# Optimization experiments

Hardware: AMD Instinct MI355X
Metric: run time of the kernel (lower is better)

The kernel has to match this reference:

```python
import jax, jax.numpy as jnp
import numpy as np
from jax import lax

B, NQ, C = 2, 1024, 2048
H, DH = 16, 128
G, CD = 4, 512          # off_grps, off_dim = C // G
LR, HR = 24, 72         # low-res grid side, high-res grid side
INTER = 64
K = LR * LR             # sampled K/V tokens (grid_size == lr_size)


def setup_inputs() -> dict:
    key = jax.random.key(0)
    ks = jax.random.split(key, 16)
    s = 0.02
    d = {}
    d['hidden_states'] = jax.random.normal(ks[0], (B, NQ, C), jnp.float32)
    d['image_hd'] = jax.random.normal(ks[1], (B, HR * HR, C), jnp.float32)
    d['wq'] = jax.random.normal(ks[2], (C, C), jnp.float32) * s
    d['wk'] = jax.random.normal(ks[3], (C, C), jnp.float32) * s
    d['wv'] = jax.random.normal(ks[4], (C, C), jnp.float32) * s
    d['wo'] = jax.random.normal(ks[5], (C, C), jnp.float32) * s
    d['conv_dw_w'] = jax.random.normal(ks[6], (CD, 1, 3, 3), jnp.float32) * s
    d['ln1_w'] = jnp.ones((CD,), jnp.float32)
    d['ln1_b'] = jnp.zeros((CD,), jnp.float32)
    d['conv_lr_proj_w'] = jax.random.normal(ks[7], (INTER, CD), jnp.float32) * s
    d['proj_int_w'] = jax.random.normal(ks[8], (INTER, CD), jnp.float32) * s
    d['proj_int_b'] = jnp.zeros((INTER,), jnp.float32)
    d['ln2_w'] = jnp.ones((INTER,), jnp.float32)
    d['ln2_b'] = jnp.zeros((INTER,), jnp.float32)
    d['conv_off_w'] = jax.random.normal(ks[9], (2, INTER), jnp.float32) * s
    d['k_hd_w'] = jax.random.normal(ks[10], (C, C), jnp.float32) * s
    d['k_hd_b'] = jnp.zeros((C,), jnp.float32)
    d['v_hd_w'] = jax.random.normal(ks[11], (C, C), jnp.float32) * s
    d['v_hd_b'] = jnp.zeros((C,), jnp.float32)
    return d


def _ln_channels(x, w, b, eps=1e-5):
    # LayerNorm2d: normalize over channel axis of [N, C, H, W]
    mu = jnp.mean(x, axis=1, keepdims=True)
    var = jnp.var(x, axis=1, keepdims=True)
    xn = (x - mu) * lax.rsqrt(var + eps)
    return xn * w[None, :, None, None] + b[None, :, None, None]


def _tokens_to_grid(x, S):
    # [B, S*S, C] -> [B*G, CD, S, S]  (group channels like einops '(b) (h w) (g c) -> (b g) c h w')
    return x.reshape(B, S, S, G, CD).transpose(0, 3, 4, 1, 2).reshape(B * G, CD, S, S)


def _bilinear_sample(img, grid):
    # img [N, C, Hh, Wh]; grid [N, K, 2] (x, y) normalized to [-1, 1], align_corners=True
    N, Cc, Hh, Wh = img.shape
    x = (grid[..., 0] + 1.0) * 0.5 * (Wh - 1)
    y = (grid[..., 1] + 1.0) * 0.5 * (Hh - 1)
    x0f, y0f = jnp.floor(x), jnp.floor(y)
    wx = (x - x0f)[:, None, :]
    wy = (y - y0f)[:, None, :]
    x0 = jnp.clip(x0f.astype(jnp.int32), 0, Wh - 1)
    x1 = jnp.clip(x0 + 1, 0, Wh - 1)
    y0 = jnp.clip(y0f.astype(jnp.int32), 0, Hh - 1)
    y1 = jnp.clip(y0 + 1, 0, Hh - 1)
    imgf = img.reshape(N, Cc, Hh * Wh)
    gather = jax.vmap(lambda im, ix: im[:, ix])  # ([C,HW],[K]) -> [C,K]
    v00 = gather(imgf, y0 * Wh + x0)
    v01 = gather(imgf, y0 * Wh + x1)
    v10 = gather(imgf, y1 * Wh + x0)
    v11 = gather(imgf, y1 * Wh + x1)
    return (v00 * (1 - wx) * (1 - wy) + v01 * wx * (1 - wy)
            + v10 * (1 - wx) * wy + v11 * wx * wy)  # [N, C, K]


def _ref_grid():
    # normalized reference points as in _grid_generate (centers / (S-1) * 2 - 1)
    yy = (jnp.linspace(0.5, LR - 0.5, LR) / (LR - 1.0)) * 2.0 - 1.0
    xx = (jnp.linspace(0.5, LR - 0.5, LR) / (LR - 1.0)) * 2.0 - 1.0
    gy, gx = jnp.meshgrid(yy, xx, indexing='ij')
    return jnp.stack([gx, gy], axis=-1).reshape(K, 2)  # (x, y)


def reference(hidden_states, image_hd, wq, wk, wv, wo, conv_dw_w, ln1_w, ln1_b,
              conv_lr_proj_w, proj_int_w, proj_int_b, ln2_w, ln2_b, conv_off_w,
              k_hd_w, k_hd_b, v_hd_w, v_hd_b):
    # ---- QKV on the full sequence ----
    q = hidden_states @ wq.T
    k_txt = hidden_states @ wk.T
    v_txt = hidden_states @ wv.T

    # ---- offset network on LR image tokens (first LR*LR tokens) ----
    lr = _tokens_to_grid(hidden_states[:, :K, :], LR)          # [B*G, CD, LR, LR]
    x = lax.conv_general_dilated(lr, conv_dw_w, (1, 1), 'SAME',
                                 feature_group_count=CD,
                                 dimension_numbers=('NCHW', 'OIHW', 'NCHW'))
    x = jax.nn.silu(x)
    x = _ln_channels(x, ln1_w, ln1_b)
    x = jnp.einsum('nchw,oc->nohw', x, conv_lr_proj_w)          # 1x1 conv -> [B*G, INTER, LR, LR]
    # intention gate from spatially pooled group features
    pooled = jnp.mean(lr, axis=(2, 3))                          # [B*G, CD]
    gate = jax.nn.sigmoid(pooled @ proj_int_w.T + proj_int_b)   # [B*G, INTER]
    x = x * gate[:, :, None, None]
    x = _ln_channels(x, ln2_w, ln2_b)
    off = jnp.einsum('nchw,oc->nohw', x, conv_off_w)            # [B*G, 2, LR, LR]
    off = off.transpose(0, 2, 3, 1).reshape(B * G, K, 2)        # (x, y)
    pos = jnp.tanh(_ref_grid()[None] + off)                     # sampling locs in [-1, 1]

    # ---- deformable gather from HD features ----
    hd = _tokens_to_grid(image_hd, HR)                          # [B*G, CD, HR, HR]
    samp = _bilinear_sample(hd, pos)                            # [B*G, CD, K]
    samp = samp.reshape(B, G, CD, K).transpose(0, 3, 1, 2).reshape(B, K, C)
    k_hd = samp @ k_hd_w.T + k_hd_b
    v_hd = samp @ v_hd_w.T + v_hd_b

    # ---- attention: causal over text tokens, HD tokens fully visible ----
    k_all = jnp.concatenate([k_txt, k_hd], axis=1)              # [B, NQ+K, C]
    v_all = jnp.concatenate([v_txt, v_hd], axis=1)
    qh = q.reshape(B, NQ, H, DH).transpose(0, 2, 1, 3)
    kh = k_all.reshape(B, NQ + K, H, DH).transpose(0, 2, 1, 3)
    vh = v_all.reshape(B, NQ + K, H, DH).transpose(0, 2, 1, 3)
    scores = jnp.einsum('bhqd,bhkd->bhqk', qh, kh) / jnp.sqrt(jnp.float32(DH))
    col = jnp.arange(NQ + K)
    row = jnp.arange(NQ)
    allow = (col[None, :] >= NQ) | (col[None, :] <= row[:, None])
    scores = jnp.where(allow[None, None], scores, jnp.float32(-1e9))
    attn = jax.nn.softmax(scores, axis=-1)
    out = jnp.einsum('bhqk,bhkd->bhqd', attn, vh)
    out = out.transpose(0, 2, 1, 3).reshape(B, NQ, C)
    return out @ wo.T
```

## Files before the change

kernel.cpp:

```cpp
#include <hip/hip_runtime.h>

typedef unsigned short u16;
typedef unsigned int u32;
typedef __attribute__((ext_vector_type(8))) short bf8;
typedef __attribute__((ext_vector_type(4))) float f4;
typedef __attribute__((ext_vector_type(4))) unsigned short us4;

constexpr int B = 2;
constexpr int NQ = 1024;
constexpr int C = 2048;
constexpr int DH = 128;
constexpr int G = 4;
constexpr int CD = 512;
constexpr int LR = 24;
constexpr int HR = 72;
constexpr int INTER = 64;
constexpr int K = LR * LR;
constexpr int NKV = NQ + K;

#define MFMA16(a, b, c) __builtin_amdgcn_mfma_f32_16x16x32_bf16(a, b, c, 0, 0, 0)
#define GLDS(g, l)                                                         \
  __builtin_amdgcn_global_load_lds(                                        \
      (const __attribute__((address_space(1))) void*)(g),                  \
      (__attribute__((address_space(3))) void*)(l), 16, 0, 0)
#define SB()                               \
  do {                                     \
    __builtin_amdgcn_sched_barrier(0);     \
    __builtin_amdgcn_s_barrier();          \
    __builtin_amdgcn_sched_barrier(0);     \
  } while (0)
#define WVM(n)                                              \
  do {                                                      \
    asm volatile("s_waitcnt vmcnt(" #n ")" ::: "memory");   \
    __builtin_amdgcn_sched_barrier(0);                      \
  } while (0)

__device__ __forceinline__ u16 f2bf1(float f) {
  u32 u = __float_as_uint(f);
  u32 r = (u + 0x7fffu + ((u >> 16) & 1u)) >> 16;
  return (u16)r;
}

__global__ __launch_bounds__(256) void f2bf_k9(
    const float* __restrict__ s0, const float* __restrict__ s1,
    const float* __restrict__ s2, const float* __restrict__ s3,
    const float* __restrict__ s4, const float* __restrict__ s5,
    const float* __restrict__ s6, const float* __restrict__ plrw,
    const float* __restrict__ cdw, u16* __restrict__ d0, u16* __restrict__ d1,
    u16* __restrict__ d2, u16* __restrict__ d3, u16* __restrict__ d4,
    u16* __restrict__ d5, u16* __restrict__ d6, float* __restrict__ wt,
    float* __restrict__ x1, float* __restrict__ pooled) {
  __shared__ float SH[32 * 577];
  const int y = blockIdx.y;
  const int t = threadIdx.x;
  if (y == 7) {
    if (blockIdx.x >= 128) return;
    const int idx = blockIdx.x * 256 + t;
    wt[idx] = plrw[(idx & 63) * 512 + (idx >> 6)];
    return;
  }
  if (y == 8) {
    if (blockIdx.x >= 128) return;
    const int n = blockIdx.x >> 4, cg = blockIdx.x & 15;
    const int b = n >> 2, g = n & 3;
    const int c0 = cg * 32;
    {
      const int c = t & 31, pr = t >> 5;
      const float* src = s0 + (size_t)b * 1024 * 2048 + g * 512 + c0 + c;
#pragma unroll 4
      for (int j = 0; j < 72; ++j) {
        const int p = j * 8 + pr;
        SH[c * 577 + p] = src[(size_t)p * 2048];
      }
    }
    __syncthreads();
    {
      const int c = t >> 3, seg = t & 7;
      float s = 0.f;
      for (int i = 0; i < 72; ++i) s += SH[c * 577 + seg * 72 + i];
      s += __shfl_xor(s, 1);
      s += __shfl_xor(s, 2);
      s += __shfl_xor(s, 4);
      if (seg == 0) pooled[n * 512 + c0 + c] = s * (1.f / 576.f);
    }
    const size_t base_out = (size_t)(n * 512 + c0) * 576;
    for (int j = 0; j < 72; ++j) {
      const int idx = j * 256 + t;
      const int c = idx / 576, p = idx - c * 576;
      const int yy0 = p / 24, xx0 = p - yy0 * 24;
      const float* wp = cdw + (c0 + c) * 9;
      float s = 0.f;
#pragma unroll
      for (int dy = -1; dy <= 1; ++dy)
#pragma unroll
        for (int dx = -1; dx <= 1; ++dx) {
          const int yy = yy0 + dy, xx = xx0 + dx;
          if (yy < 0 || yy >= 24 || xx < 0 || xx >= 24) continue;
          s += SH[c * 577 + yy * 24 + xx] * wp[(dy + 1) * 3 + dx + 1];
        }
      x1[base_out + idx] = s / (1.f + expf(-s));
    }
    return;
  }
  const float* s;
  u16* d;
  switch (y) {
    case 0: s = s0; d = d0; break;
    case 1: s = s1; d = d1; break;
    case 2: s = s2; d = d2; break;
    case 3: s = s3; d = d3; break;
    case 4: s = s4; d = d4; break;
    case 5: s = s5; d = d5; break;
    default: s = s6; d = d6; break;
  }
  if (y < 5) {
    u16* L = (u16*)SH;
    const int pc = blockIdx.x;
    const int mb = pc >> 5, kb = pc & 31;
    const int rin = t >> 2, c0 = (t & 3) * 16;
    const float* src = s + (size_t)(mb * 64 + rin) * 2048 + kb * 64 + c0;
#pragma unroll
    for (int j = 0; j < 16; j += 4) {
      float4 v = *(const float4*)(src + j);
      L[rin * 68 + c0 + j] = f2bf1(v.x);
      L[rin * 68 + c0 + j + 1] = f2bf1(v.y);
      L[rin * 68 + c0 + j + 2] = f2bf1(v.z);
      L[rin * 68 + c0 + j + 3] = f2bf1(v.w);
    }
    __syncthreads();
    u16* dst = d + (size_t)pc * 4096 + t * 16;
#pragma unroll
    for (int gg = 0; gg < 2; ++gg) {
      const int g = t * 2 + gg;
      const int rh = g & 15, ks2 = (g >> 4) & 3, kc = (g >> 6) & 1, fr = g >> 7;
      const int row = fr * 16 + rh, cc = kc * 32 + ks2 * 8;
      us4 o0, o1;
      o0.x = L[row * 68 + cc];     o0.y = L[row * 68 + cc + 1];
      o0.z = L[row * 68 + cc + 2]; o0.w = L[row * 68 + cc + 3];
      o1.x = L[row * 68 + cc + 4]; o1.y = L[row * 68 + cc + 5];
      o1.z = L[row * 68 + cc + 6]; o1.w = L[row * 68 + cc + 7];
      *(us4*)(dst + gg * 8) = o0;
      *(us4*)(dst + gg * 8 + 4) = o1;
    }
  } else {
    const size_t i0 = ((size_t)blockIdx.x * 256 + t) * 16;
#pragma unroll
    for (int j = 0; j < 16; j += 4) {
      float4 v = *(const float4*)(s + i0 + j);
      us4 o;
      o.x = f2bf1(v.x); o.y = f2bf1(v.y); o.z = f2bf1(v.z); o.w = f2bf1(v.w);
      *(us4*)(d + i0 + j) = o;
    }
  }
}

__global__ __launch_bounds__(512, 2) void gemm_fused(
    const u16* __restrict__ Ast, const u16* __restrict__ Wq,
    const u16* __restrict__ Wk, const u16* __restrict__ Wv,
    const u16* __restrict__ samp, const u16* __restrict__ khw,
    const u16* __restrict__ vhw, const float* __restrict__ khb,
    const float* __restrict__ vhb, u16* __restrict__ outq,
    u16* __restrict__ kg, u16* __restrict__ vg) {
  __shared__ u16 As[2][4][4096];
  __shared__ u16 Bs[2][4][4096];
  const int tid = threadIdx.x, lane = tid & 63, w = tid >> 6;
  const int ks = lane >> 4, r = lane & 15;
  const int bid = blockIdx.x;

  if (bid < 192) {
    const int wm = w >> 2, wn = w & 3;
    const int swz = (bid & 7) * 24 + (bid >> 3);
    const int mt = swz / 24, nt = swz % 24;
    const u16* Wst = (nt < 8) ? Wq : (nt < 16) ? Wk : Wv;
    const int nb0 = (nt & 7) * 4;
    const int mb0 = mt * 4;

#define ST_A03(bi, kt)                                                        \
  do {                                                                        \
    GLDS(Ast + ((size_t)(mb0 + 0) * 32 + (kt)) * 4096 + tid * 8,              \
         &As[bi][0][tid * 8]);                                                \
    GLDS(Ast + ((size_t)(mb0 + 2) * 32 + (kt)) * 4096 + tid * 8,              \
         &As[bi][2][tid * 8]);                                                \
  } while (0)
#define ST_A47(bi, kt)                                                        \
  do {                                                                        \
    GLDS(Ast + ((size_t)(mb0 + 1) * 32 + (kt)) * 4096 + tid * 8,              \
         &As[bi][1][tid * 8]);                                                \
    GLDS(Ast + ((size_t)(mb0 + 3) * 32 + (kt)) * 4096 + tid * 8,              \
         &As[bi][3][tid * 8]);                                                \
  } while (0)
#define ST_B01(bi, kt)                                                        \
  do {                                                                        \
    GLDS(Wst + ((size_t)(nb0 + 0) * 32 + (kt)) * 4096 + tid * 8,              \
         &Bs[bi][0][tid * 8]);                                                \
    GLDS(Wst + ((size_t)(nb0 + 1) * 32 + (kt)) * 4096 + tid * 8,              \
         &Bs[bi][1][tid * 8]);                                                \
  } while (0)
#define ST_B23(bi, kt)                                                        \
  do {                                                                        \
    GLDS(Wst + ((size_t)(nb0 + 2) * 32 + (kt)) * 4096 + tid * 8,              \
         &Bs[bi][2][tid * 8]);                                                \
    GLDS(Wst + ((size_t)(nb0 + 3) * 32 + (kt)) * 4096 + tid * 8,              \
         &Bs[bi][3][tid * 8]);                                                \
  } while (0)
#define RD_A(dst, bi, half, kc)                                               \
  _Pragma("unroll") for (int i2 = 0; i2 < 4; ++i2) dst[i2] =                  \
      *(const bf8*)(&As[bi][wm * 2 + (half)]                                  \
                       [((i2 * 2 + (kc)) * 4 + ks) * 128 + r * 8]);
#define RD_B(dst, bi, kc)                                                     \
  _Pragma("unroll") for (int j2 = 0; j2 < 4; ++j2) dst[j2] =                  \
      *(const bf8*)(&Bs[bi][wn][((j2 * 2 + (kc)) * 4 + ks) * 128 + r * 8]);
#define MM(ACC, AF, BF)                                                       \
  do {                                                                        \
    __builtin_amdgcn_s_setprio(1);                                            \
    _Pragma("unroll") for (int i3 = 0; i3 < 4; ++i3)                          \
        _Pragma("unroll") for (int j3 = 0; j3 < 4; ++j3) ACC[i3][j3] =        \
            MFMA16(AF[i3], BF[j3], ACC[i3][j3]);                              \
    __builtin_amdgcn_s_setprio(0);                                            \
  } while (0)

    f4 accA[4][4], accB[4][4];
#pragma unroll
    for (int i = 0; i < 4; ++i)
#pragma unroll
      for (int j = 0; j < 4; ++j) {
        accA[i][j] = f4{0.f, 0.f, 0.f, 0.f};
        accB[i][j] = f4{0.f, 0.f, 0.f, 0.f};
      }
    bf8 af[4], b0[4], b1[4];

    ST_A03(0, 0); ST_B01(0, 0); ST_B23(0, 0); ST_A47(0, 0);
    ST_A03(1, 1); ST_B01(1, 1);
    WVM(6);
    SB();

    for (int t = 0; t < 32; ++t) {
      const int buf = t & 1;
      RD_A(af, buf, 0, 0);
      RD_B(b0, buf, 0);
      if (t + 1 < 32) ST_B23(buf ^ 1, t + 1);
      SB();
      MM(accA, af, b0);
      SB();
      RD_A(af, buf, 0, 1);
      RD_B(b1, buf, 1);
      if (t + 1 < 32) ST_A47(buf ^ 1, t + 1);
      SB();
      MM(accA, af, b1);
      if (t + 1 < 32) { WVM(8); } else { WVM(0); }
      SB();
      RD_A(af, buf, 1, 0);
      if (t + 2 < 32) ST_A03(buf, t + 2);
      SB();
      MM(accB, af, b0);
      SB();
      RD_A(af, buf, 1, 1);
      if (t + 2 < 32) ST_B01(buf, t + 2);
      SB();
      MM(accB, af, b1);
      if (t + 2 < 32) { WVM(6); } else if (t + 1 < 32) { WVM(2); }
      SB();
    }

#define EPI(ACC, HALF)                                                        \
  _Pragma("unroll") for (int i = 0; i < 4; ++i)                               \
      _Pragma("unroll") for (int j = 0; j < 4; ++j)                           \
          _Pragma("unroll") for (int rr = 0; rr < 4; ++rr) {                  \
    const int m = mt * 256 + wm * 128 + (HALF)*64 + i * 16 + ks * 4 + rr;     \
    const int n = nt * 256 + wn * 64 + j * 16 + r;                            \
    const float v = ACC[i][j][rr];                                            \
    const int sel = n >> 11, nn = n & 2047, hh = nn >> 7, dd = nn & 127;      \
    const int bb = m >> 10, qq = m & 1023;                                    \
    const u16 bv = f2bf1(v);                                                  \
    if (sel == 0) {                                                           \
      outq[(size_t)m * 2048 + nn] = bv;                                       \
    } else if (sel == 1) {                                                    \
      kg[(((size_t)(bb * 16 + hh) * 50 + (qq >> 5)) * 16 + (dd >> 3)) * 256 + \
         (qq & 31) * 8 + (dd & 7)] = bv;                                      \
    } else {                                                                  \
      vg[((size_t)(bb * 16 + hh) * 200 + (qq >> 3)) * 1024 + dd * 8 +         \
         (qq & 7)] = bv;                                                      \
    }                                                                         \
  }
    EPI(accA, 0)
    EPI(accB, 1)
#undef EPI
  } else {
    const int hb = bid - 192;
    const int mt = hb >> 4, nb = hb & 15;
    const int m0 = mt * 128, n0l = nb * 128;
    const int srow = lane >> 2, scol = (lane & 3) * 8;
    const int wh = w & 3;
    const int wr = wh >> 1, wc = wh & 1;
    const bool is_v = (w >= 4);
    const u16* Wp = is_v ? vhw : khw;
    const float* bias = is_v ? vhb : khb;

#define HDST(bi, k0)                                                          \
  do {                                                                        \
    GLDS(samp + (size_t)(m0 + w * 16 + srow) * 2048 + scol + (k0),            \
         &As[bi][0][w * 512 + lane * 8]);                                     \
    GLDS(Wp + (size_t)(n0l + wh * 32 + srow) * 2048 + scol + (k0),            \
         &Bs[bi][is_v ? 1 : 0][wh * 1024 + lane * 8]);                        \
    GLDS(Wp + (size_t)(n0l + wh * 32 + 16 + srow) * 2048 + scol + (k0),       \
         &Bs[bi][is_v ? 1 : 0][wh * 1024 + 512 + lane * 8]);                  \
  } while (0)

    f4 acc[4][4];
#pragma unroll
    for (int i = 0; i < 4; ++i)
#pragma unroll
      for (int j = 0; j < 4; ++j) acc[i][j] = f4{0.f, 0.f, 0.f, 0.f};
    const int koff = ks * 8;
    const int arow = wr * 64 + r, brow = wc * 64 + r;

    HDST(0, 0);
    int cur = 0;
    for (int k0 = 0; k0 < 2048; k0 += 32) {
      SB();
      if (k0 + 32 < 2048) {
        HDST(cur ^ 1, k0 + 32);
        WVM(3);
      } else {
        WVM(0);
      }
      SB();
      bf8 af2[4], bw[4];
#pragma unroll
      for (int i = 0; i < 4; ++i)
        af2[i] = *(const bf8*)(&As[cur][0][(arow + i * 16) * 32 + koff]);
#pragma unroll
      for (int j = 0; j < 4; ++j)
        bw[j] =
            *(const bf8*)(&Bs[cur][is_v ? 1 : 0][(brow + j * 16) * 32 + koff]);
      __builtin_amdgcn_s_setprio(1);
#pragma unroll
      for (int i = 0; i < 4; ++i)
#pragma unroll
        for (int j = 0; j < 4; ++j)
          acc[i][j] = MFMA16(af2[i], bw[j], acc[i][j]);
      __builtin_amdgcn_s_setprio(0);
      cur ^= 1;
    }
#undef HDST
    const int rbase = ks * 4;
#pragma unroll
    for (int i = 0; i < 4; ++i) {
#pragma unroll
      for (int j = 0; j < 4; ++j) {
        const int nn = n0l + wc * 64 + j * 16 + r;
        const int hh = nn >> 7, dd = nn & 127;
#pragma unroll
        for (int rr = 0; rr < 4; ++rr) {
          const int m = m0 + wr * 64 + i * 16 + rbase + rr;
          const int bb = m / 576;
          const int kv = 1024 + (m - bb * 576);
          const u16 bv = f2bf1(acc[i][j][rr] + bias[nn]);
          if (!is_v) {
            kg[(((size_t)(bb * 16 + hh) * 50 + (kv >> 5)) * 16 + (dd >> 3)) *
                   256 +
               (kv & 31) * 8 + (dd & 7)] = bv;
          } else {
            vg[((size_t)(bb * 16 + hh) * 200 + (kv >> 3)) * 1024 + dd * 8 +
               (kv & 7)] = bv;
          }
        }
      }
    }
  }
}

__global__ __launch_bounds__(256) void gemm_out_st(const u16* __restrict__ Ast2,
                                                   const u16* __restrict__ Wst,
                                                   float* __restrict__ outf) {
  __shared__ u16 As2[2][2][4096];
  __shared__ u16 Ws2[2][2][4096];
  const int tid = threadIdx.x, lane = tid & 63, w = tid >> 6;
  const int wr = w >> 1, wc = w & 1;
  const int ks = lane >> 4, r = lane & 15;
  const int mt = blockIdx.y, nt = blockIdx.x;

#define OST(bi, kt)                                                           \
  do {                                                                        \
    const size_t a0 = ((size_t)(mt * 2 + 0) * 32 + (kt)) * 4096;              \
    const size_t a1 = ((size_t)(mt * 2 + 1) * 32 + (kt)) * 4096;              \
    const size_t w0 = ((size_t)(nt * 2 + 0) * 32 + (kt)) * 4096;              \
    const size_t w1 = ((size_t)(nt * 2 + 1) * 32 + (kt)) * 4096;              \
    GLDS(Ast2 + a0 + tid * 8, &As2[bi][0][tid * 8]);                          \
    GLDS(Ast2 + a0 + 2048 + tid * 8, &As2[bi][0][2048 + tid * 8]);            \
    GLDS(Ast2 + a1 + tid * 8, &As2[bi][1][tid * 8]);                          \
    GLDS(Ast2 + a1 + 2048 + tid * 8, &As2[bi][1][2048 + tid * 8]);            \
    GLDS(Wst + w0 + tid * 8, &Ws2[bi][0][tid * 8]);                           \
    GLDS(Wst + w0 + 2048 + tid * 8, &Ws2[bi][0][2048 + tid * 8]);             \
    GLDS(Wst + w1 + tid * 8, &Ws2[bi][1][tid * 8]);                           \
    GLDS(Wst + w1 + 2048 + tid * 8, &Ws2[bi][1][2048 + tid * 8]);             \
  } while (0)

  f4 acc[4][4];
#pragma unroll
  for (int i = 0; i < 4; ++i)
#pragma unroll
    for (int j = 0; j < 4; ++j) acc[i][j] = f4{0.f, 0.f, 0.f, 0.f};

  OST(0, 0);
  int cur = 0;
  for (int kt = 0; kt < 32; ++kt) {
    SB();
    if (kt + 1 < 32) {
      OST(cur ^ 1, kt + 1);
      WVM(8);
    } else {
      WVM(0);
    }
    SB();
#pragma unroll
    for (int kc = 0; kc < 2; ++kc) {
      bf8 a_[4], b_[4];
#pragma unroll
      for (int i = 0; i < 4; ++i)
        a_[i] = *(const bf8*)(&As2[cur][wr][((i * 2 + kc) * 4 + ks) * 128 +
                                            r * 8]);
#pragma unroll
      for (int j = 0; j < 4; ++j)
        b_[j] = *(const bf8*)(&Ws2[cur][wc][((j * 2 + kc) * 4 + ks) * 128 +
                                            r * 8]);
      __builtin_amdgcn_s_setprio(1);
#pragma unroll
      for (int i = 0; i < 4; ++i)
#pragma unroll
        for (int j = 0; j < 4; ++j)
          acc[i][j] = MFMA16(a_[i], b_[j], acc[i][j]);
      __builtin_amdgcn_s_setprio(0);
    }
    cur ^= 1;
  }
#undef OST
#pragma unroll
  for (int i = 0; i < 4; ++i)
#pragma unroll
    for (int j = 0; j < 4; ++j) {
      const int n = nt * 128 + wc * 64 + j * 16 + r;
#pragma unroll
      for (int rr = 0; rr < 4; ++rr) {
        const int m = mt * 128 + wr * 64 + i * 16 + ks * 4 + rr;
        outf[(size_t)m * 2048 + n] = acc[i][j][rr];
      }
    }
}

__global__ __launch_bounds__(256) void lnproj_gate(
    const float* __restrict__ x1, const float* __restrict__ ln1w,
    const float* __restrict__ ln1b, const float* __restrict__ wt,
    const float* __restrict__ pooled, const float* __restrict__ piw,
    const float* __restrict__ pib, float* __restrict__ x2,
    float* __restrict__ gate) {
  __shared__ float Xs[512][68];
  __shared__ float rs[4][64], rss[4][64];
  const int bidx = blockIdx.x;
  const int t = threadIdx.x;
  if (bidx >= 72) {
    const int idx = (bidx - 72) * 256 + t;
    const int n = idx >> 6, o = idx & 63;
    const float* pb = pooled + n * 512;
    const float* wb = piw + o * 512;
    float s = pib[o];
    for (int c = 0; c < 512; ++c) s += pb[c] * wb[c];
    gate[idx] = 1.f / (1.f + expf(-s));
    return;
  }
  const int n = bidx / 9, pc = bidx % 9;
  const int p0 = pc * 64;
  {
    const int pl = t & 63, c4 = t >> 6;
    const float* src = x1 + (size_t)n * 512 * 576 + p0 + pl;
#pragma unroll 4
    for (int j = 0; j < 128; ++j) {
      const int c = j * 4 + c4;
      Xs[c][pl] = src[(size_t)c * 576];
    }
  }
  __syncthreads();
  {
    const int pl = t & 63, q = t >> 6;
    float s = 0.f, ss = 0.f;
    for (int c = q * 128; c < q * 128 + 128; ++c) {
      const float v = Xs[c][pl];
      s += v;
      ss += v * v;
    }
    rs[q][pl] = s;
    rss[q][pl] = ss;
    __syncthreads();
    const float S = rs[0][pl] + rs[1][pl] + rs[2][pl] + rs[3][pl];
    const float SS = rss[0][pl] + rss[1][pl] + rss[2][pl] + rss[3][pl];
    const float mean = S * (1.f / 512.f);
    const float inv = rsqrtf(SS * (1.f / 512.f) - mean * mean + 1e-5f);
    for (int c = q * 128; c < q * 128 + 128; ++c)
      Xs[c][pl] = (Xs[c][pl] - mean) * inv * ln1w[c] + ln1b[c];
  }
  __syncthreads();
  {
    const int o4 = (t & 15) * 4, pl0 = (t >> 4) * 4;
    float acc[4][4] = {};
    for (int c = 0; c < 512; ++c) {
      const f4 xv = *(const f4*)(&Xs[c][pl0]);
      const f4 wv = *(const f4*)(&wt[c * 64 + o4]);
#pragma unroll
      for (int i = 0; i < 4; ++i)
#pragma unroll
        for (int j = 0; j < 4; ++j) acc[i][j] += wv[i] * xv[j];
    }
#pragma unroll
    for (int i = 0; i < 4; ++i) {
      f4 ov;
      ov[0] = acc[i][0]; ov[1] = acc[i][1];
      ov[2] = acc[i][2]; ov[3] = acc[i][3];
      *(f4*)(&x2[(size_t)(n * 64 + o4 + i) * 576 + p0 + pl0]) = ov;
    }
  }
}

__global__ __launch_bounds__(256) void pos_sample(
    const float* __restrict__ x2, const float* __restrict__ gate,
    const float* __restrict__ ln2w, const float* __restrict__ ln2b,
    const float* __restrict__ offw, const float* __restrict__ img,
    u16* __restrict__ samp) {
  const int bk = blockIdx.x;
  const int b = bk / K, k = bk % K;
  __shared__ int s_idx[G][4];
  __shared__ float s_w[G][4];
  const int t = threadIdx.x;
  const int g = t >> 6, lane = t & 63;
  {
    const int n = b * G + g;
    float v = x2[((size_t)n * INTER + lane) * K + k] * gate[n * INTER + lane];
    float s = v, ss = v * v;
    for (int o = 32; o; o >>= 1) {
      s += __shfl_xor(s, o);
      ss += __shfl_xor(ss, o);
    }
    const float mean = s * (1.f / INTER);
    const float var = ss * (1.f / INTER) - mean * mean;
    const float xn = (v - mean) * rsqrtf(var + 1e-5f) * ln2w[lane] + ln2b[lane];
    float ox = xn * offw[lane];
    float oy = xn * offw[INTER + lane];
    for (int o = 32; o; o >>= 1) {
      ox += __shfl_xor(ox, o);
      oy += __shfl_xor(oy, o);
    }
    if (lane == 0) {
      const int yi = k / LR, xi = k % LR;
      const float rx = (xi + 0.5f) / 23.f * 2.f - 1.f;
      const float ry = (yi + 0.5f) / 23.f * 2.f - 1.f;
      const float px = tanhf(rx + ox), py = tanhf(ry + oy);
      const float x = (px + 1.f) * 0.5f * (HR - 1);
      const float y = (py + 1.f) * 0.5f * (HR - 1);
      const float x0f = floorf(x), y0f = floorf(y);
      const float wx = x - x0f, wy = y - y0f;
      const int x0 = min(max((int)x0f, 0), HR - 1);
      const int x1 = min(x0 + 1, HR - 1);
      const int y0 = min(max((int)y0f, 0), HR - 1);
      const int y1 = min(y0 + 1, HR - 1);
      s_idx[g][0] = y0 * HR + x0;
      s_idx[g][1] = y0 * HR + x1;
      s_idx[g][2] = y1 * HR + x0;
      s_idx[g][3] = y1 * HR + x1;
      s_w[g][0] = (1.f - wx) * (1.f - wy);
      s_w[g][1] = wx * (1.f - wy);
      s_w[g][2] = (1.f - wx) * wy;
      s_w[g][3] = wx * wy;
    }
  }
  __syncthreads();
  const float* ib = img + (size_t)b * HR * HR * C;
  u16* ob = samp + ((size_t)b * K + k) * C;
  for (int ch = t; ch < C; ch += 256) {
    const int gg = ch >> 9;
    float v = s_w[gg][0] * ib[(size_t)s_idx[gg][0] * C + ch] +
              s_w[gg][1] * ib[(size_t)s_idx[gg][1] * C + ch] +
              s_w[gg][2] * ib[(size_t)s_idx[gg][2] * C + ch] +
              s_w[gg][3] * ib[(size_t)s_idx[gg][3] * C + ch];
    ob[ch] = f2bf1(v);
  }
}

__global__ __launch_bounds__(256) void attn_part(
    const u16* __restrict__ qb, const u16* __restrict__ kg,
    const u16* __restrict__ vg, float* __restrict__ oA,
    float* __restrict__ oB, float* __restrict__ mlA,
    float* __restrict__ mlB) {
  const int i = blockIdx.x;
  const int fam = i >> 9;
  const int r9 = i & 511;
  int bh, qblk;
  if (fam == 0) {
    const int pair = r9 & 255, half = r9 >> 8;
    bh = pair & 31;
    const int q8 = pair >> 5;
    qblk = half ? (15 - q8) : q8;
  } else {
    bh = r9 & 31;
    qblk = r9 >> 5;
  }
  const int b = bh >> 4, h = bh & 15;
  const int q0 = qblk * 64;
  const int tid = threadIdx.x, lane = tid & 63, w = tid >> 6;
  const int qw = q0 + w * 16;
  const int col = lane & 15, kpart = lane >> 4, rbase = kpart * 4;
  __shared__ u16 Ks[2][4096];
  __shared__ u16 Vs[2][4096];
  __shared__ u16 Pl[4][16 * 40];
  float* oacc = fam ? oB : oA;
  float* ml = fam ? mlB : mlA;
  bf8 qf[4];
  {
    const u16* qp =
        qb + (size_t)(b * 1024 + qw + col) * 2048 + h * 128 + kpart * 8;
#pragma unroll
    for (int dc = 0; dc < 4; ++dc) qf[dc] = *(const bf8*)(qp + dc * 32);
  }
  f4 o[8];
#pragma unroll
  for (int df = 0; df < 8; ++df) o[df] = f4{0.f, 0.f, 0.f, 0.f};
  float m_r[4] = {-1e30f, -1e30f, -1e30f, -1e30f};
  float l_p[4] = {0.f, 0.f, 0.f, 0.f};
  const float scale = 0.08838834764831845f;
  const int nt = fam ? 18 : ((q0 + 64) >> 5);
  const int kvadd = fam ? 1024 : 0;
  const u16* kbh = kg + (size_t)bh * (NKV * 128);
  const u16* vbh = vg + (size_t)bh * (NKV * 128);
  u16* pw = &Pl[w][0];

#define ASTAGE(bi, kv0)                                                       \
  do {                                                                        \
    const u16* gk = kbh + (size_t)((kv0) >> 5) * 4096 + w * 1024 + lane * 8;  \
    GLDS(gk, &Ks[bi][w * 1024 + lane * 8]);                                   \
    GLDS(gk + 512, &Ks[bi][w * 1024 + 512 + lane * 8]);                       \
    const u16* gv = vbh + (size_t)((kv0) >> 3) * 1024 + w * 1024 + lane * 8;  \
    GLDS(gv, &Vs[bi][w * 1024 + lane * 8]);                                   \
    GLDS(gv + 512, &Vs[bi][w * 1024 + 512 + lane * 8]);                       \
  } while (0)

  ASTAGE(0, kvadd);
  int cur = 0;
  for (int t = 0; t < nt; ++t) {
    const int kv0 = kvadd + (t << 5);
    SB();
    if (t + 1 < nt) {
      ASTAGE(cur ^ 1, kvadd + ((t + 1) << 5));
      WVM(4);
    } else {
      WVM(0);
    }
    SB();
    const u16* ksb = &Ks[cur][0];
    const u16* vsb = &Vs[cur][0];
    f4 s0 = {0.f, 0.f, 0.f, 0.f}, s1 = {0.f, 0.f, 0.f, 0.f};
    __builtin_amdgcn_s_setprio(1);
#pragma unroll
    for (int dc = 0; dc < 4; ++dc) {
      const int dblk = dc * 4 + kpart;
      bf8 k0f = *(const bf8*)(ksb + (dblk * 32 + col) * 8);
      bf8 k1f = *(const bf8*)(ksb + (dblk * 32 + 16 + col) * 8);
      s0 = MFMA16(qf[dc], k0f, s0);
      s1 = MFMA16(qf[dc], k1f, s1);
    }
    __builtin_amdgcn_s_setprio(0);
    float sa[4], sc[4], loc[4], p0[4], p1[4];
    bool grow = false;
    const bool need_mask = (fam == 0) && (kv0 + 31 > qw);
#pragma unroll
    for (int rr = 0; rr < 4; ++rr) {
      float a = s0[rr] * scale, c2 = s1[rr] * scale;
      if (need_mask) {
        const int qg = qw + rbase + rr;
        if (kv0 + col > qg) a = -1e30f;
        if (kv0 + 16 + col > qg) c2 = -1e30f;
      }
      sa[rr] = a; sc[rr] = c2;
      loc[rr] = fmaxf(a, c2);
      grow |= (loc[rr] > m_r[rr] + 8.f);
    }
    if (__any(grow)) {
      float fr[4];
#pragma unroll
      for (int rr = 0; rr < 4; ++rr) {
        float mx = loc[rr];
        mx = fmaxf(mx, __shfl_xor(mx, 1));
        mx = fmaxf(mx, __shfl_xor(mx, 2));
        mx = fmaxf(mx, __shfl_xor(mx, 4));
        mx = fmaxf(mx, __shfl_xor(mx, 8));
        const float mn = fmaxf(m_r[rr], mx);
        fr[rr] = __expf(m_r[rr] - mn);
        m_r[rr] = mn;
        p0[rr] = __expf(sa[rr] - mn);
        p1[rr] = __expf(sc[rr] - mn);
        l_p[rr] = l_p[rr] * fr[rr] + p0[rr] + p1[rr];
      }
#pragma unroll
      for (int df = 0; df < 8; ++df) {
        o[df][0] *= fr[0]; o[df][1] *= fr[1];
        o[df][2] *= fr[2]; o[df][3] *= fr[3];
      }
    } else {
#pragma unroll
      for (int rr = 0; rr < 4; ++rr) {
        p0[rr] = __expf(sa[rr] - m_r[rr]);
        p1[rr] = __expf(sc[rr] - m_r[rr]);
        l_p[rr] += p0[rr] + p1[rr];
      }
    }
#pragma unroll
    for (int rr = 0; rr < 4; ++rr) {
      pw[(rbase + rr) * 40 + col] = f2bf1(p0[rr]);
      pw[(rbase + rr) * 40 + 16 + col] = f2bf1(p1[rr]);
    }
    bf8 pa = *(const bf8*)(pw + col * 40 + kpart * 8);
    __builtin_amdgcn_s_setprio(1);
#pragma unroll
    for (int df = 0; df < 8; ++df) {
      bf8 vf = *(const bf8*)(vsb + (kpart * 128 + df * 16 + col) * 8);
      o[df] = MFMA16(pa, vf, o[df]);
    }
    __builtin_amdgcn_s_setprio(0);
    cur ^= 1;
  }
#undef ASTAGE
  float l_r[4];
#pragma unroll
  for (int rr = 0; rr < 4; ++rr) {
    float ps = l_p[rr];
    ps += __shfl_xor(ps, 1);
    ps += __shfl_xor(ps, 2);
    ps += __shfl_xor(ps, 4);
    ps += __shfl_xor(ps, 8);
    l_r[rr] = ps;
  }
  float* orow = oacc + (size_t)(bh * 1024 + qw + rbase) * 128 + col;
#pragma unroll
  for (int df = 0; df < 8; ++df)
#pragma unroll
    for (int rr = 0; rr < 4; ++rr)
      orow[(size_t)rr * 128 + df * 16] = o[df][rr];
  if (col == 0) {
#pragma unroll
    for (int rr = 0; rr < 4; ++rr) {
      const int row = bh * 1024 + qw + rbase + rr;
      ml[row * 2] = m_r[rr];
      ml[row * 2 + 1] = l_r[rr];
    }
  }
}

__global__ __launch_bounds__(256) void attn_merge(
    const float* __restrict__ oA, const float* __restrict__ mlA,
    const float* __restrict__ oB, const float* __restrict__ mlB,
    u16* __restrict__ aob_st) {
  const int gid = blockIdx.x * 256 + threadIdx.x;
  const int row = gid >> 5;
  const int d0 = (gid & 31) * 4;
  const float mA = mlA[row * 2], lA = mlA[row * 2 + 1];
  const float mB = mlB[row * 2], lB = mlB[row * 2 + 1];
  const float m = fmaxf(mA, mB);
  const float wA = __expf(mA - m), wB = __expf(mB - m);
  const float inv = 1.f / (lA * wA + lB * wB);
  const f4 a = *(const f4*)(oA + (size_t)row * 128 + d0);
  const f4 c = *(const f4*)(oB + (size_t)row * 128 + d0);
  const int bh = row >> 10, q = row & 1023;
  const int bb = bh >> 4, h = bh & 15;
  const int mm = bb * 1024 + q;
  const int col = h * 128 + d0;
  const int mb = mm >> 6, fr = (mm >> 4) & 3, r = mm & 15;
  const int kb = col >> 6, kc = (col >> 5) & 1, ks = (col >> 3) & 3,
            j0 = col & 7;
  u16* dst = aob_st + ((size_t)(mb * 32 + kb)) * 4096 +
             (((fr * 2 + kc) * 4 + ks) * 16 + r) * 8 + j0;
  us4 ov;
  ov.x = f2bf1((a[0] * wA + c[0] * wB) * inv);
  ov.y = f2bf1((a[1] * wA + c[1] * wB) * inv);
  ov.z = f2bf1((a[2] * wA + c[2] * wB) * inv);
  ov.w = f2bf1((a[3] * wA + c[3] * wB) * inv);
  *(us4*)dst = ov;
}

extern "C" void kernel_launch(void* const* d_in, const int* in_sizes, int n_in,
                              void* d_out, int out_size, void* d_ws,
                              size_t ws_size, hipStream_t stream) {
  const float* hs = (const float*)d_in[0];
  const float* img = (const float*)d_in[1];
  const float* wq = (const float*)d_in[2];
  const float* wk = (const float*)d_in[3];
  const float* wv = (const float*)d_in[4];
  const float* wo = (const float*)d_in[5];
  const float* cdw = (const float*)d_in[6];
  const float* ln1w = (const float*)d_in[7];
  const float* ln1b = (const float*)d_in[8];
  const float* plrw = (const float*)d_in[9];
  const float* piw = (const float*)d_in[10];
  const float* pib = (const float*)d_in[11];
  const float* ln2w = (const float*)d_in[12];
  const float* ln2b = (const float*)d_in[13];
  const float* offw = (const float*)d_in[14];
  const float* khw = (const float*)d_in[15];
  const float* khb = (const float*)d_in[16];
  const float* vhw = (const float*)d_in[17];
  const float* vhb = (const float*)d_in[18];
  float* outp = (float*)d_out;

  u16* wsp = (u16*)d_ws;
  const size_t SZ = 4194304;
  u16* hs_st = wsp;
  u16* wq_st = wsp + SZ;
  u16* wk_st = wsp + 2 * SZ;
  u16* wv_st = wsp + 3 * SZ;
  u16* wo_st = wsp + 4 * SZ;
  u16* khw_bf = wsp + 5 * SZ;
  u16* vhw_bf = wsp + 6 * SZ;
  u16* qb_bf = wsp + 7 * SZ;
  u16* samp_bf = wsp + 8 * SZ;
  u16* kg = wsp + 8 * SZ + 2359296;
  u16* vg = kg + 6553600;
  float* x1b = (float*)kg + 2359296;
  float* x2b = x1b + 2359296;
  float* poolb = x2b + 294912;
  float* gb = poolb + 4096;
  float* posb = (float*)(vg + 6553600);
  float* mlA = posb + 9216;
  float* mlB = mlA + 65536;
  float* wtb = mlB + 65536;
  float* oA = (float*)(wsp + 2 * SZ);
  float* oB = (float*)(wsp + 5 * SZ);
  u16* aob_st = wq_st;

  dim3 blk(256);
  f2bf_k9<<<dim3(1024, 9), blk, 0, stream>>>(
      hs, wq, wk, wv, wo, khw, vhw, plrw, cdw, hs_st, wq_st, wk_st, wv_st,
      wo_st, khw_bf, vhw_bf, wtb, x1b, poolb);
  lnproj_gate<<<dim3(74), blk, 0, stream>>>(x1b, ln1w, ln1b, wtb, poolb, piw,
                                            pib, x2b, gb);
  pos_sample<<<dim3(B * K), blk, 0, stream>>>(x2b, gb, ln2w, ln2b, offw, img,
                                              samp_bf);
  gemm_fused<<<dim3(336), dim3(512), 0, stream>>>(
      hs_st, wq_st, wk_st, wv_st, samp_bf, khw_bf, vhw_bf, khb, vhb, qb_bf,
      kg, vg);
  attn_part<<<dim3(1024), blk, 0, stream>>>(qb_bf, kg, vg, oA, oB, mlA, mlB);
  attn_merge<<<dim3(4096), blk, 0, stream>>>(oA, mlA, oB, mlB, aob_st);
  gemm_out_st<<<dim3(16, 16), blk, 0, stream>>>(aob_st, wo_st, outp);
}
```

Baseline: 346.1 us.

## Unify GEMMs into one templated tile kernel and fuse attention halves

Replaces the 512-thread 256x256 QKV GEMM and separate HD and output GEMMs with a single templated 256-thread, 128x128-tile kernel that uses XCD-aware block mapping. All weights, including the HD K/V weights, are now pre-staged into the swizzled tile layout, and the sampler writes directly in that layout. Attention now processes text and HD keys in one pass per block, which removes the split partial outputs and the separate merge kernel. The aim is fewer launches, less intermediate fp32 traffic and better load balance, at the cost of smaller tiles with less operand reuse and longer per-block attention loops.

Result: slower. 420.7 us (+21.5%).

```diff
diff --git a/kernel.cpp b/kernel.cpp
--- a/kernel.cpp
+++ b/kernel.cpp
@@ -113,246 +113,175 @@
     case 5: s = s5; d = d5; break;
     default: s = s6; d = d6; break;
   }
-  if (y < 5) {
-    u16* L = (u16*)SH;
-    const int pc = blockIdx.x;
-    const int mb = pc >> 5, kb = pc & 31;
-    const int rin = t >> 2, c0 = (t & 3) * 16;
-    const float* src = s + (size_t)(mb * 64 + rin) * 2048 + kb * 64 + c0;
-#pragma unroll
-    for (int j = 0; j < 16; j += 4) {
-      float4 v = *(const float4*)(src + j);
-      L[rin * 68 + c0 + j] = f2bf1(v.x);
-      L[rin * 68 + c0 + j + 1] = f2bf1(v.y);
-      L[rin * 68 + c0 + j + 2] = f2bf1(v.z);
-      L[rin * 68 + c0 + j + 3] = f2bf1(v.w);
-    }
-    __syncthreads();
-    u16* dst = d + (size_t)pc * 4096 + t * 16;
-#pragma unroll
-    for (int gg = 0; gg < 2; ++gg) {
-      const int g = t * 2 + gg;
-      const int rh = g & 15, ks2 = (g >> 4) & 3, kc = (g >> 6) & 1, fr = g >> 7;
-      const int row = fr * 16 + rh, cc = kc * 32 + ks2 * 8;
-      us4 o0, o1;
-      o0.x = L[row * 68 + cc];     o0.y = L[row * 68 + cc + 1];
-      o0.z = L[row * 68 + cc + 2]; o0.w = L[row * 68 + cc + 3];
-      o1.x = L[row * 68 + cc + 4]; o1.y = L[row * 68 + cc + 5];
-      o1.z = L[row * 68 + cc + 6]; o1.w = L[row * 68 + cc + 7];
-      *(us4*)(dst + gg * 8) = o0;
-      *(us4*)(dst + gg * 8 + 4) = o1;
-    }
-  } else {
-    const size_t i0 = ((size_t)blockIdx.x * 256 + t) * 16;
-#pragma unroll
-    for (int j = 0; j < 16; j += 4) {
-      float4 v = *(const float4*)(s + i0 + j);
-      us4 o;
-      o.x = f2bf1(v.x); o.y = f2bf1(v.y); o.z = f2bf1(v.z); o.w = f2bf1(v.w);
-      *(us4*)(d + i0 + j) = o;
-    }
+  u16* L = (u16*)SH;
+  const int pc = blockIdx.x;
+  const int mb = pc >> 5, kb = pc & 31;
+  const int rin = t >> 2, c0 = (t & 3) * 16;
+  const float* src = s + (size_t)(mb * 64 + rin) * 2048 + kb * 64 + c0;
+#pragma unroll
+  for (int j = 0; j < 16; j += 4) {
+    float4 v = *(const float4*)(src + j);
+    L[rin * 68 + c0 + j] = f2bf1(v.x);
+    L[rin * 68 + c0 + j + 1] = f2bf1(v.y);
+    L[rin * 68 + c0 + j + 2] = f2bf1(v.z);
+    L[rin * 68 + c0 + j + 3] = f2bf1(v.w);
+  }
+  __syncthreads();
+  u16* dst = d + (size_t)pc * 4096 + t * 16;
+#pragma unroll
+  for (int gg = 0; gg < 2; ++gg) {
+    const int g = t * 2 + gg;
+    const int rh = g & 15, ks2 = (g >> 4) & 3, kc = (g >> 6) & 1, fr = g >> 7;
+    const int row = fr * 16 + rh, cc = kc * 32 + ks2 * 8;
+    us4 o0, o1;
+    o0.x = L[row * 68 + cc];     o0.y = L[row * 68 + cc + 1];
+    o0.z = L[row * 68 + cc + 2]; o0.w = L[row * 68 + cc + 3];
+    o1.x = L[row * 68 + cc + 4]; o1.y = L[row * 68 + cc + 5];
+    o1.z = L[row * 68 + cc + 6]; o1.w = L[row * 68 + cc + 7];
+    *(us4*)(dst + gg * 8) = o0;
+    *(us4*)(dst + gg * 8 + 4) = o1;
   }
 }
 
-__global__ __launch_bounds__(512, 2) void gemm_fused(
-    const u16* __restrict__ Ast, const u16* __restrict__ Wq,
-    const u16* __restrict__ Wk, const u16* __restrict__ Wv,
-    const u16* __restrict__ samp, const u16* __restrict__ khw,
+template <int MODE>
+__global__ __launch_bounds__(256) void gemm_all(
+    const u16* __restrict__ Ast, const u16* __restrict__ W0,
+    const u16* __restrict__ W1, const u16* __restrict__ W2,
+    const u16* __restrict__ sampst, const u16* __restrict__ khw,
     const u16* __restrict__ vhw, const float* __restrict__ khb,
     const float* __restrict__ vhb, u16* __restrict__ outq,
-    u16* __restrict__ kg, u16* __restrict__ vg) {
-  __shared__ u16 As[2][4][4096];
-  __shared__ u16 Bs[2][4][4096];
+    u16* __restrict__ kg, u16* __restrict__ vg, float* __restrict__ outf) {
+  __shared__ u16 As[2][4096];
+  __shared__ u16 Bs[2][4096];
   const int tid = threadIdx.x, lane = tid & 63, w = tid >> 6;
-  const int ks = lane >> 4, r = lane & 15;
-  const int bid = blockIdx.x;
-
-  if (bid < 192) {
-    const int wm = w >> 2, wn = w & 3;
-    const int swz = (bid & 7) * 24 + (bid >> 3);
-    const int mt = swz / 24, nt = swz % 24;
-    const u16* Wst = (nt < 8) ? Wq : (nt < 16) ? Wk : Wv;
-    const int nb0 = (nt & 7) * 4;
-    const int mb0 = mt * 4;
-
-#define ST_A03(bi, kt)                                                        \
-  do {                                                                        \
-    GLDS(Ast + ((size_t)(mb0 + 0) * 32 + (kt)) * 4096 + tid * 8,              \
-         &As[bi][0][tid * 8]);                                                \
-    GLDS(Ast + ((size_t)(mb0 + 2) * 32 + (kt)) * 4096 + tid * 8,              \
-         &As[bi][2][tid * 8]);                                                \
+  const int wr = w >> 1, wc = w & 1;
+  const int ksl = lane >> 4, rl = lane & 15;
+  int mt, nt;
+  const u16 *Ap, *Wp;
+  bool isHD = false;
+  if (MODE == 0) {
+    if (blockIdx.x < 768) {
+      const int xcd = blockIdx.x & 7, idx = blockIdx.x >> 3;
+      mt = (xcd >> 2) * 8 + idx / 12;
+      nt = (xcd & 3) * 12 + idx % 12;
+      Ap = Ast;
+      Wp = (nt < 16) ? W0 : (nt < 32) ? W1 : W2;
+    } else {
+      isHD = true;
+      const int hb = blockIdx.x - 768, xcd = hb & 7, idx = hb >> 3;
+      mt = idx >> 2;
+      nt = xcd * 4 + (idx & 3);
+      Ap = sampst;
+      Wp = (nt < 16) ? khw : vhw;
+    }
+  } else {
+    const int xcd = blockIdx.x & 7, idx = blockIdx.x >> 3;
+    mt = (xcd >> 2) * 8 + idx / 4;
+    nt = (xcd & 3) * 4 + idx % 4;
+    Ap = Ast;
+    Wp = W0;
+  }
+  const int ma0 = mt * 2;
+  const int nb0 = (nt & 15) * 2;
+
+#define GST(dstArr, srcBase, tb0, kt)                                      \
+  do {                                                                     \
+    const int kb_ = (kt) >> 1, kc_ = (kt) & 1;                             \
+    _Pragma("unroll") for (int r2 = 0; r2 < 2; ++r2) {                     \
+      const int run = r2 * 4 + w;                                          \
+      GLDS(srcBase + ((size_t)((tb0) + (run >> 2)) * 32 + kb_) * 4096 +    \
+               (run & 3) * 1024 + kc_ * 512 + lane * 8,                    \
+           &dstArr[run * 512 + lane * 8]);                                 \
+    }                                                                      \
   } while (0)
-#define ST_A47(bi, kt)                                                        \
-  do {                                                                        \
-    GLDS(Ast + ((size_t)(mb0 + 1) * 32 + (kt)) * 4096 + tid * 8,              \
-         &As[bi][1][tid * 8]);                                                \
-    GLDS(Ast + ((size_t)(mb0 + 3) * 32 + (kt)) * 4096 + tid * 8,              \
-         &As[bi][3][tid * 8]);                                                \
-  } while (0)
-#define ST_B01(bi, kt)                                                        \
-  do {                                                                        \
-    GLDS(Wst + ((size_t)(nb0 + 0) * 32 + (kt)) * 4096 + tid * 8,              \
-         &Bs[bi][0][tid * 8]);                                                \
-    GLDS(Wst + ((size_t)(nb0 + 1) * 32 + (kt)) * 4096 + tid * 8,              \
-         &Bs[bi][1][tid * 8]);                                                \
-  } while (0)
-#define ST_B23(bi, kt)                                                        \
-  do {                                                                        \
-    GLDS(Wst + ((size_t)(nb0 + 2) * 32 + (kt)) * 4096 + tid * 8,              \
-         &Bs[bi][2][tid * 8]);                                                \
-    GLDS(Wst + ((size_t)(nb0 + 3) * 32 + (kt)) * 4096 + tid * 8,              \
-         &Bs[bi][3][tid * 8]);                                                \
-  } while (0)
-#define RD_A(dst, bi, half, kc)                                               \
-  _Pragma("unroll") for (int i2 = 0; i2 < 4; ++i2) dst[i2] =                  \
-      *(const bf8*)(&As[bi][wm * 2 + (half)]                                  \
-                       [((i2 * 2 + (kc)) * 4 + ks) * 128 + r * 8]);
-#define RD_B(dst, bi, kc)                                                     \
-  _Pragma("unroll") for (int j2 = 0; j2 < 4; ++j2) dst[j2] =                  \
-      *(const bf8*)(&Bs[bi][wn][((j2 * 2 + (kc)) * 4 + ks) * 128 + r * 8]);
-#define MM(ACC, AF, BF)                                                       \
-  do {                                                                        \
-    __builtin_amdgcn_s_setprio(1);                                            \
-    _Pragma("unroll") for (int i3 = 0; i3 < 4; ++i3)                          \
-        _Pragma("unroll") for (int j3 = 0; j3 < 4; ++j3) ACC[i3][j3] =        \
-            MFMA16(AF[i3], BF[j3], ACC[i3][j3]);                              \
-    __builtin_amdgcn_s_setprio(0);                                            \
-  } while (0)
-
-    f4 accA[4][4], accB[4][4];
+
+  f4 acc[4][4];
+#pragma unroll
+  for (int i = 0; i < 4; ++i)
+#pragma unroll
+    for (int j = 0; j < 4; ++j) acc[i][j] = f4{0.f, 0.f, 0.f, 0.f};
+
+  GST(As[0], Ap, ma0, 0);
+  GST(Bs[0], Wp, nb0, 0);
+  int cur = 0;
+  for (int kt = 0; kt < 64; ++kt) {
+    SB();
+    if (kt + 1 < 64) {
+      GST(As[cur ^ 1], Ap, ma0, kt + 1);
+      GST(Bs[cur ^ 1], Wp, nb0, kt + 1);
+      WVM(4);
+    } else {
+      WVM(0);
+    }
+    SB();
+    bf8 af[4], bw[4];
 #pragma unroll
     for (int i = 0; i < 4; ++i)
+      af[i] = *(const bf8*)(&As[cur][(wr * 4 + i) * 512 + ksl * 128 + rl * 8]);
+#pragma unroll
+    for (int j = 0; j < 4; ++j)
+      bw[j] = *(const bf8*)(&Bs[cur][(wc * 4 + j) * 512 + ksl * 128 + rl * 8]);
+    __builtin_amdgcn_s_setprio(1);
+#pragma unroll
+    for (int i = 0; i < 4; ++i)
+#pragma unroll
+      for (int j = 0; j < 4; ++j)
+        acc[i][j] = MFMA16(af[i], bw[j], acc[i][j]);
+    __builtin_amdgcn_s_setprio(0);
+    cur ^= 1;
+  }
+#undef GST
+
+  const int rbase = ksl * 4;
+  if (MODE == 1) {
+#pragma unroll
+    for (int i = 0; i < 4; ++i)
 #pragma unroll
       for (int j = 0; j < 4; ++j) {
-        accA[i][j] = f4{0.f, 0.f, 0.f, 0.f};
-        accB[i][j] = f4{0.f, 0.f, 0.f, 0.f};
-      }
-    bf8 af[4], b0[4], b1[4];
-
-    ST_A03(0, 0); ST_B01(0, 0); ST_B23(0, 0); ST_A47(0, 0);
-    ST_A03(1, 1); ST_B01(1, 1);
-    WVM(6);
-    SB();
-
-    for (int t = 0; t < 32; ++t) {
-      const int buf = t & 1;
-      RD_A(af, buf, 0, 0);
-      RD_B(b0, buf, 0);
-      if (t + 1 < 32) ST_B23(buf ^ 1, t + 1);
-      SB();
-      MM(accA, af, b0);
-      SB();
-      RD_A(af, buf, 0, 1);
-      RD_B(b1, buf, 1);
-      if (t + 1 < 32) ST_A47(buf ^ 1, t + 1);
-      SB();
-      MM(accA, af, b1);
-      if (t + 1 < 32) { WVM(8); } else { WVM(0); }
-      SB();
-      RD_A(af, buf, 1, 0);
-      if (t + 2 < 32) ST_A03(buf, t + 2);
-      SB();
-      MM(accB, af, b0);
-      SB();
-      RD_A(af, buf, 1, 1);
-      if (t + 2 < 32) ST_B01(buf, t + 2);
-      SB();
-      MM(accB, af, b1);
-      if (t + 2 < 32) { WVM(6); } else if (t + 1 < 32) { WVM(2); }
-      SB();
-    }
-
-#define EPI(ACC, HALF)                                                        \
-  _Pragma("unroll") for (int i = 0; i < 4; ++i)                               \
-      _Pragma("unroll") for (int j = 0; j < 4; ++j)                           \
-          _Pragma("unroll") for (int rr = 0; rr < 4; ++rr) {                  \
-    const int m = mt * 256 + wm * 128 + (HALF)*64 + i * 16 + ks * 4 + rr;     \
-    const int n = nt * 256 + wn * 64 + j * 16 + r;                            \
-    const float v = ACC[i][j][rr];                                            \
-    const int sel = n >> 11, nn = n & 2047, hh = nn >> 7, dd = nn & 127;      \
-    const int bb = m >> 10, qq = m & 1023;                                    \
-    const u16 bv = f2bf1(v);                                                  \
-    if (sel == 0) {                                                           \
-      outq[(size_t)m * 2048 + nn] = bv;                                       \
-    } else if (sel == 1) {                                                    \
-      kg[(((size_t)(bb * 16 + hh) * 50 + (qq >> 5)) * 16 + (dd >> 3)) * 256 + \
-         (qq & 31) * 8 + (dd & 7)] = bv;                                      \
-    } else {                                                                  \
-      vg[((size_t)(bb * 16 + hh) * 200 + (qq >> 3)) * 1024 + dd * 8 +         \
-         (qq & 7)] = bv;                                                      \
-    }                                                                         \
-  }
-    EPI(accA, 0)
-    EPI(accB, 1)
-#undef EPI
+        const int n = nt * 128 + wc * 64 + j * 16 + rl;
+#pragma unroll
+        for (int rr = 0; rr < 4; ++rr) {
+          const int m = mt * 128 + wr * 64 + i * 16 + rbase + rr;
+          outf[(size_t)m * 2048 + n] = acc[i][j][rr];
+        }
+      }
+  } else if (!isHD) {
+    const int sel = nt >> 4;
+#pragma unroll
+    for (int i = 0; i < 4; ++i)
+#pragma unroll
+      for (int j = 0; j < 4; ++j) {
+        const int n2 = (nt & 15) * 128 + wc * 64 + j * 16 + rl;
+        const int hh = n2 >> 7, dd = n2 & 127;
+#pragma unroll
+        for (int rr = 0; rr < 4; ++rr) {
+          const int m = mt * 128 + wr * 64 + i * 16 + rbase + rr;
+          const int bb = m >> 10, qq = m & 1023;
+          const u16 bv = f2bf1(acc[i][j][rr]);
+          if (sel == 0) {
+            outq[(size_t)m * 2048 + n2] = bv;
+          } else if (sel == 1) {
+            kg[(((size_t)(bb * 16 + hh) * 50 + (qq >> 5)) * 16 + (dd >> 3)) *
+                   256 +
+               (qq & 31) * 8 + (dd & 7)] = bv;
+          } else {
+            vg[((size_t)(bb * 16 + hh) * 200 + (qq >> 3)) * 1024 + dd * 8 +
+               (qq & 7)] = bv;
+          }
+        }
+      }
   } else {
-    const int hb = bid - 192;
-    const int mt = hb >> 4, nb = hb & 15;
-    const int m0 = mt * 128, n0l = nb * 128;
-    const int srow = lane >> 2, scol = (lane & 3) * 8;
-    const int wh = w & 3;
-    const int wr = wh >> 1, wc = wh & 1;
-    const bool is_v = (w >= 4);
-    const u16* Wp = is_v ? vhw : khw;
+    const bool is_v = (nt >= 16);
     const float* bias = is_v ? vhb : khb;
-
-#define HDST(bi, k0)                                                          \
-  do {                                                                        \
-    GLDS(samp + (size_t)(m0 + w * 16 + srow) * 2048 + scol + (k0),            \
-         &As[bi][0][w * 512 + lane * 8]);                                     \
-    GLDS(Wp + (size_t)(n0l + wh * 32 + srow) * 2048 + scol + (k0),            \
-         &Bs[bi][is_v ? 1 : 0][wh * 1024 + lane * 8]);                        \
-    GLDS(Wp + (size_t)(n0l + wh * 32 + 16 + srow) * 2048 + scol + (k0),       \
-         &Bs[bi][is_v ? 1 : 0][wh * 1024 + 512 + lane * 8]);                  \
-  } while (0)
-
-    f4 acc[4][4];
 #pragma unroll
     for (int i = 0; i < 4; ++i)
 #pragma unroll
-      for (int j = 0; j < 4; ++j) acc[i][j] = f4{0.f, 0.f, 0.f, 0.f};
-    const int koff = ks * 8;
-    const int arow = wr * 64 + r, brow = wc * 64 + r;
-
-    HDST(0, 0);
-    int cur = 0;
-    for (int k0 = 0; k0 < 2048; k0 += 32) {
-      SB();
-      if (k0 + 32 < 2048) {
-        HDST(cur ^ 1, k0 + 32);
-        WVM(3);
-      } else {
-        WVM(0);
-      }
-      SB();
-      bf8 af2[4], bw[4];
-#pragma unroll
-      for (int i = 0; i < 4; ++i)
-        af2[i] = *(const bf8*)(&As[cur][0][(arow + i * 16) * 32 + koff]);
-#pragma unroll
-      for (int j = 0; j < 4; ++j)
-        bw[j] =
-            *(const bf8*)(&Bs[cur][is_v ? 1 : 0][(brow + j * 16) * 32 + koff]);
-      __builtin_amdgcn_s_setprio(1);
-#pragma unroll
-      for (int i = 0; i < 4; ++i)
-#pragma unroll
-        for (int j = 0; j < 4; ++j)
-          acc[i][j] = MFMA16(af2[i], bw[j], acc[i][j]);
-      __builtin_amdgcn_s_setprio(0);
-      cur ^= 1;
-    }
-#undef HDST
-    const int rbase = ks * 4;
-#pragma unroll
-    for (int i = 0; i < 4; ++i) {
-#pragma unroll
       for (int j = 0; j < 4; ++j) {
-        const int nn = n0l + wc * 64 + j * 16 + r;
+        const int nn = (nt & 15) * 128 + wc * 64 + j * 16 + rl;
         const int hh = nn >> 7, dd = nn & 127;
 #pragma unroll
         for (int rr = 0; rr < 4; ++rr) {
-          const int m = m0 + wr * 64 + i * 16 + rbase + rr;
+          const int m = mt * 128 + wr * 64 + i * 16 + rbase + rr;
           const int bb = m / 576;
           const int kv = 1024 + (m - bb * 576);
           const u16 bv = f2bf1(acc[i][j][rr] + bias[nn]);
@@ -366,86 +295,7 @@
           }
         }
       }
-    }
-  }
-}
-
-__global__ __launch_bounds__(256) void gemm_out_st(const u16* __restrict__ Ast2,
-                                                   const u16* __restrict__ Wst,
-                                                   float* __restrict__ outf) {
-  __shared__ u16 As2[2][2][4096];
-  __shared__ u16 Ws2[2][2][4096];
-  const int tid = threadIdx.x, lane = tid & 63, w = tid >> 6;
-  const int wr = w >> 1, wc = w & 1;
-  const int ks = lane >> 4, r = lane & 15;
-  const int mt = blockIdx.y, nt = blockIdx.x;
-
-#define OST(bi, kt)                                                           \
-  do {                                                                        \
-    const size_t a0 = ((size_t)(mt * 2 + 0) * 32 + (kt)) * 4096;              \
-    const size_t a1 = ((size_t)(mt * 2 + 1) * 32 + (kt)) * 4096;              \
-    const size_t w0 = ((size_t)(nt * 2 + 0) * 32 + (kt)) * 4096;              \
-    const size_t w1 = ((size_t)(nt * 2 + 1) * 32 + (kt)) * 4096;              \
-    GLDS(Ast2 + a0 + tid * 8, &As2[bi][0][tid * 8]);                          \
-    GLDS(Ast2 + a0 + 2048 + tid * 8, &As2[bi][0][2048 + tid * 8]);            \
-    GLDS(Ast2 + a1 + tid * 8, &As2[bi][1][tid * 8]);                          \
-    GLDS(Ast2 + a1 + 2048 + tid * 8, &As2[bi][1][2048 + tid * 8]);            \
-    GLDS(Wst + w0 + tid * 8, &Ws2[bi][0][tid * 8]);                           \
-    GLDS(Wst + w0 + 2048 + tid * 8, &Ws2[bi][0][2048 + tid * 8]);             \
-    GLDS(Wst + w1 + tid * 8, &Ws2[bi][1][tid * 8]);                           \
-    GLDS(Wst + w1 + 2048 + tid * 8, &Ws2[bi][1][2048 + tid * 8]);             \
-  } while (0)
-
-  f4 acc[4][4];
-#pragma unroll
-  for (int i = 0; i < 4; ++i)
-#pragma unroll
-    for (int j = 0; j < 4; ++j) acc[i][j] = f4{0.f, 0.f, 0.f, 0.f};
-
-  OST(0, 0);
-  int cur = 0;
-  for (int kt = 0; kt < 32; ++kt) {
-    SB();
-    if (kt + 1 < 32) {
-      OST(cur ^ 1, kt + 1);
-      WVM(8);
-    } else {
-      WVM(0);
-    }
-    SB();
-#pragma unroll
-    for (int kc = 0; kc < 2; ++kc) {
-      bf8 a_[4], b_[4];
-#pragma unroll
-      for (int i = 0; i < 4; ++i)
-        a_[i] = *(const bf8*)(&As2[cur][wr][((i * 2 + kc) * 4 + ks) * 128 +
-                                            r * 8]);
-#pragma unroll
-      for (int j = 0; j < 4; ++j)
-        b_[j] = *(const bf8*)(&Ws2[cur][wc][((j * 2 + kc) * 4 + ks) * 128 +
-                                            r * 8]);
-      __builtin_amdgcn_s_setprio(1);
-#pragma unroll
-      for (int i = 0; i < 4; ++i)
-#pragma unroll
-        for (int j = 0; j < 4; ++j)
-          acc[i][j] = MFMA16(a_[i], b_[j], acc[i][j]);
-      __builtin_amdgcn_s_setprio(0);
-    }
-    cur ^= 1;
-  }
-#undef OST
-#pragma unroll
-  for (int i = 0; i < 4; ++i)
-#pragma unroll
-    for (int j = 0; j < 4; ++j) {
-      const int n = nt * 128 + wc * 64 + j * 16 + r;
-#pragma unroll
-      for (int rr = 0; rr < 4; ++rr) {
-        const int m = mt * 128 + wr * 64 + i * 16 + ks * 4 + rr;
-        outf[(size_t)m * 2048 + n] = acc[i][j][rr];
-      }
-    }
+  }
 }
 
 __global__ __launch_bounds__(256) void lnproj_gate(
@@ -524,7 +374,7 @@
     const float* __restrict__ x2, const float* __restrict__ gate,
     const float* __restrict__ ln2w, const float* __restrict__ ln2b,
     const float* __restrict__ offw, const float* __restrict__ img,
-    u16* __restrict__ samp) {
+    u16* __restrict__ sampst) {
   const int bk = blockIdx.x;
   const int b = bk / K, k = bk % K;
   __shared__ int s_idx[G][4];
@@ -572,36 +422,41 @@
     }
   }
   __syncthreads();
-  const float* ib = img + (size_t)b * HR * HR * C;
-  u16* ob = samp + ((size_t)b * K + k) * C;
-  for (int ch = t; ch < C; ch += 256) {
-    const int gg = ch >> 9;
-    float v = s_w[gg][0] * ib[(size_t)s_idx[gg][0] * C + ch] +
-              s_w[gg][1] * ib[(size_t)s_idx[gg][1] * C + ch] +
-              s_w[gg][2] * ib[(size_t)s_idx[gg][2] * C + ch] +
-              s_w[gg][3] * ib[(size_t)s_idx[gg][3] * C + ch];
-    ob[ch] = f2bf1(v);
-  }
+  const int m = b * 576 + k;
+  const int mb = m >> 6, fr = (m >> 4) & 3, r = m & 15;
+  const int ch0 = t * 8;
+  const int gg = ch0 >> 9;
+  const float* ib = img + (size_t)b * HR * HR * C + ch0;
+  float v[8];
+#pragma unroll
+  for (int j = 0; j < 8; ++j) v[j] = 0.f;
+#pragma unroll
+  for (int q = 0; q < 4; ++q) {
+    const float wq_ = s_w[gg][q];
+    const float* p = ib + (size_t)s_idx[gg][q] * C;
+    const float4 a = *(const float4*)p;
+    const float4 c = *(const float4*)(p + 4);
+    v[0] += wq_ * a.x; v[1] += wq_ * a.y; v[2] += wq_ * a.z; v[3] += wq_ * a.w;
+    v[4] += wq_ * c.x; v[5] += wq_ * c.y; v[6] += wq_ * c.z; v[7] += wq_ * c.w;
+  }
+  const int kb = ch0 >> 6, kc = (ch0 >> 5) & 1, ks3 = (ch0 >> 3) & 3;
+  u16* dst = sampst + ((size_t)(mb * 32 + kb)) * 4096 +
+             (((fr * 2 + kc) * 4 + ks3) * 16 + r) * 8;
+  us4 o0, o1;
+  o0.x = f2bf1(v[0]); o0.y = f2bf1(v[1]); o0.z = f2bf1(v[2]); o0.w = f2bf1(v[3]);
+  o1.x = f2bf1(v[4]); o1.y = f2bf1(v[5]); o1.z = f2bf1(v[6]); o1.w = f2bf1(v[7]);
+  *(us4*)dst = o0;
+  *(us4*)(dst + 4) = o1;
 }
 
-__global__ __launch_bounds__(256) void attn_part(
+__global__ __launch_bounds__(256) void attn_u(
     const u16* __restrict__ qb, const u16* __restrict__ kg,
-    const u16* __restrict__ vg, float* __restrict__ oA,
-    float* __restrict__ oB, float* __restrict__ mlA,
-    float* __restrict__ mlB) {
+    const u16* __restrict__ vg, u16* __restrict__ aob_st) {
   const int i = blockIdx.x;
-  const int fam = i >> 9;
-  const int r9 = i & 511;
-  int bh, qblk;
-  if (fam == 0) {
-    const int pair = r9 & 255, half = r9 >> 8;
-    bh = pair & 31;
-    const int q8 = pair >> 5;
-    qblk = half ? (15 - q8) : q8;
-  } else {
-    bh = r9 & 31;
-    qblk = r9 >> 5;
-  }
+  const int pair = i & 255, half = i >> 8;
+  const int bh = pair & 31;
+  const int q8 = pair >> 5;
+  const int qblk = half ? (15 - q8) : q8;
   const int b = bh >> 4, h = bh & 15;
   const int q0 = qblk * 64;
   const int tid = threadIdx.x, lane = tid & 63, w = tid >> 6;
@@ -610,8 +465,6 @@
   __shared__ u16 Ks[2][4096];
   __shared__ u16 Vs[2][4096];
   __shared__ u16 Pl[4][16 * 40];
-  float* oacc = fam ? oB : oA;
-  float* ml = fam ? mlB : mlA;
   bf8 qf[4];
   {
     const u16* qp =
@@ -625,8 +478,8 @@
   float m_r[4] = {-1e30f, -1e30f, -1e30f, -1e30f};
   float l_p[4] = {0.f, 0.f, 0.f, 0.f};
   const float scale = 0.08838834764831845f;
-  const int nt = fam ? 18 : ((q0 + 64) >> 5);
-  const int kvadd = fam ? 1024 : 0;
+  const int nt_text = (q0 + 64) >> 5;
+  const int nt = nt_text + 18;
   const u16* kbh = kg + (size_t)bh * (NKV * 128);
   const u16* vbh = vg + (size_t)bh * (NKV * 128);
   u16* pw = &Pl[w][0];
@@ -641,13 +494,17 @@
     GLDS(gv + 512, &Vs[bi][w * 1024 + 512 + lane * 8]);                       \
   } while (0)
 
-  ASTAGE(0, kvadd);
+  ASTAGE(0, 0);
   int cur = 0;
   for (int t = 0; t < nt; ++t) {
-    const int kv0 = kvadd + (t << 5);
+    const bool is_text = t < nt_text;
+    const int kv0 = is_text ? (t << 5) : (1024 + ((t - nt_text) << 5));
     SB();
     if (t + 1 < nt) {
-      ASTAGE(cur ^ 1, kvadd + ((t + 1) << 5));
+      const int t1 = t + 1;
+      const int kv1 =
+          (t1 < nt_text) ? (t1 << 5) : (1024 + ((t1 - nt_text) << 5));
+      ASTAGE(cur ^ 1, kv1);
       WVM(4);
     } else {
       WVM(0);
@@ -668,7 +525,7 @@
     __builtin_amdgcn_s_setprio(0);
     float sa[4], sc[4], loc[4], p0[4], p1[4];
     bool grow = false;
-    const bool need_mask = (fam == 0) && (kv0 + 31 > qw);
+    const bool need_mask = is_text && (kv0 + 31 > qw);
 #pragma unroll
     for (int rr = 0; rr < 4; ++rr) {
       float a = s0[rr] * scale, c2 = s1[rr] * scale;
@@ -726,7 +583,7 @@
     cur ^= 1;
   }
 #undef ASTAGE
-  float l_r[4];
+  float inv[4];
 #pragma unroll
   for (int rr = 0; rr < 4; ++rr) {
     float ps = l_p[rr];
@@ -734,53 +591,22 @@
     ps += __shfl_xor(ps, 2);
     ps += __shfl_xor(ps, 4);
     ps += __shfl_xor(ps, 8);
-    l_r[rr] = ps;
-  }
-  float* orow = oacc + (size_t)(bh * 1024 + qw + rbase) * 128 + col;
-#pragma unroll
-  for (int df = 0; df < 8; ++df)
-#pragma unroll
-    for (int rr = 0; rr < 4; ++rr)
-      orow[(size_t)rr * 128 + df * 16] = o[df][rr];
-  if (col == 0) {
-#pragma unroll
-    for (int rr = 0; rr < 4; ++rr) {
-      const int row = bh * 1024 + qw + rbase + rr;
-      ml[row * 2] = m_r[rr];
-      ml[row * 2 + 1] = l_r[rr];
-    }
-  }
-}
-
-__global__ __launch_bounds__(256) void attn_merge(
-    const float* __restrict__ oA, const float* __restrict__ mlA,
-    const float* __restrict__ oB, const float* __restrict__ mlB,
-    u16* __restrict__ aob_st) {
-  const int gid = blockIdx.x * 256 + threadIdx.x;
-  const int row = gid >> 5;
-  const int d0 = (gid & 31) * 4;
-  const float mA = mlA[row * 2], lA = mlA[row * 2 + 1];
-  const float mB = mlB[row * 2], lB = mlB[row * 2 + 1];
-  const float m = fmaxf(mA, mB);
-  const float wA = __expf(mA - m), wB = __expf(mB - m);
-  const float inv = 1.f / (lA * wA + lB * wB);
-  const f4 a = *(const f4*)(oA + (size_t)row * 128 + d0);
-  const f4 c = *(const f4*)(oB + (size_t)row * 128 + d0);
-  const int bh = row >> 10, q = row & 1023;
-  const int bb = bh >> 4, h = bh & 15;
-  const int mm = bb * 1024 + q;
-  const int col = h * 128 + d0;
-  const int mb = mm >> 6, fr = (mm >> 4) & 3, r = mm & 15;
-  const int kb = col >> 6, kc = (col >> 5) & 1, ks = (col >> 3) & 3,
-            j0 = col & 7;
-  u16* dst = aob_st + ((size_t)(mb * 32 + kb)) * 4096 +
-             (((fr * 2 + kc) * 4 + ks) * 16 + r) * 8 + j0;
-  us4 ov;
-  ov.x = f2bf1((a[0] * wA + c[0] * wB) * inv);
-  ov.y = f2bf1((a[1] * wA + c[1] * wB) * inv);
-  ov.z = f2bf1((a[2] * wA + c[2] * wB) * inv);
-  ov.w = f2bf1((a[3] * wA + c[3] * wB) * inv);
-  *(us4*)dst = ov;
+    inv[rr] = 1.f / ps;
+  }
+#pragma unroll
+  for (int rr = 0; rr < 4; ++rr) {
+    const int m = b * 1024 + qw + rbase + rr;
+    const int mb = m >> 6, fr3 = (m >> 4) & 3, r16 = m & 15;
+#pragma unroll
+    for (int df = 0; df < 8; ++df) {
+      const int ncol = h * 128 + df * 16 + col;
+      const int kb = ncol >> 6, kc = (ncol >> 5) & 1, ks3 = (ncol >> 3) & 3,
+                j0 = ncol & 7;
+      aob_st[((size_t)(mb * 32 + kb)) * 4096 +
+             (((fr3 * 2 + kc) * 4 + ks3) * 16 + r16) * 8 + j0] =
+          f2bf1(o[df][rr] * inv[rr]);
+    }
+  }
 }
 
 extern "C" void kernel_launch(void* const* d_in, const int* in_sizes, int n_in,
@@ -814,36 +640,33 @@
   u16* wk_st = wsp + 2 * SZ;
   u16* wv_st = wsp + 3 * SZ;
   u16* wo_st = wsp + 4 * SZ;
-  u16* khw_bf = wsp + 5 * SZ;
-  u16* vhw_bf = wsp + 6 * SZ;
+  u16* khw_st = wsp + 5 * SZ;
+  u16* vhw_st = wsp + 6 * SZ;
   u16* qb_bf = wsp + 7 * SZ;
-  u16* samp_bf = wsp + 8 * SZ;
+  u16* samp_st = wsp + 8 * SZ;
   u16* kg = wsp + 8 * SZ + 2359296;
   u16* vg = kg + 6553600;
   float* x1b = (float*)kg + 2359296;
   float* x2b = x1b + 2359296;
   float* poolb = x2b + 294912;
   float* gb = poolb + 4096;
-  float* posb = (float*)(vg + 6553600);
-  float* mlA = posb + 9216;
-  float* mlB = mlA + 65536;
-  float* wtb = mlB + 65536;
-  float* oA = (float*)(wsp + 2 * SZ);
-  float* oB = (float*)(wsp + 5 * SZ);
+  float* wtb = (float*)(vg + 6553600);
   u16* aob_st = wq_st;
 
   dim3 blk(256);
   f2bf_k9<<<dim3(1024, 9), blk, 0, stream>>>(
       hs, wq, wk, wv, wo, khw, vhw, plrw, cdw, hs_st, wq_st, wk_st, wv_st,
-      wo_st, khw_bf, vhw_bf, wtb, x1b, poolb);
+      wo_st, khw_st, vhw_st, wtb, x1b, poolb);
   lnproj_gate<<<dim3(74), blk, 0, stream>>>(x1b, ln1w, ln1b, wtb, poolb, piw,
                                             pib, x2b, gb);
   pos_sample<<<dim3(B * K), blk, 0, stream>>>(x2b, gb, ln2w, ln2b, offw, img,
-                                              samp_bf);
-  gemm_fused<<<dim3(336), dim3(512), 0, stream>>>(
-      hs_st, wq_st, wk_st, wv_st, samp_bf, khw_bf, vhw_bf, khb, vhb, qb_bf,
-      kg, vg);
-  attn_part<<<dim3(1024), blk, 0, stream>>>(qb_bf, kg, vg, oA, oB, mlA, mlB);
-  attn_merge<<<dim3(4096), blk, 0, stream>>>(oA, mlA, oB, mlB, aob_st);
-  gemm_out_st<<<dim3(16, 16), blk, 0, stream>>>(aob_st, wo_st, outp);
+                                              samp_st);
+  gemm_all<0><<<dim3(1056), blk, 0, stream>>>(
+      hs_st, wq_st, wk_st, wv_st, samp_st, khw_st, vhw_st, khb, vhb, qb_bf,
+      kg, vg, nullptr);
+  attn_u<<<dim3(512), blk, 0, stream>>>(qb_bf, kg, vg, aob_st);
+  gemm_all<1><<<dim3(256), blk, 0, stream>>>(aob_st, wo_st, nullptr, nullptr,
+                                             nullptr, nullptr, nullptr,
+                                             nullptr, nullptr, nullptr,
+                                             nullptr, nullptr, outp);
 }
```
